# Optimization experiments

Measured on AMD Instinct MI355X. Metric: run time of the kernel, lower is better.

## Reference

```python
import jax, jax.numpy as jnp
import numpy as np

B, M, S, F, E, H, L = 4, 10, 1024, 128, 512, 8, 6
DH = E // H
NV, NP = 6, 3
LN_EPS = 1e-5


def _ln(x, g, b):
    mu = x.mean(-1, keepdims=True)
    var = ((x - mu) ** 2).mean(-1, keepdims=True)
    return (x - mu) * jax.lax.rsqrt(var + LN_EPS) * g + b


def setup_inputs() -> dict:
    key = jax.random.key(0)
    ks = jax.random.split(key, 24)
    sc = 0.02
    inp = {
        'features': jax.random.normal(ks[0], (B, M, S, F), jnp.float32),
        'target': jax.random.normal(ks[1], (B, S, NV), jnp.float32),
        'step_idx': jax.random.randint(ks[2], (B,), 0, 40),
        'day_of_year': jax.random.randint(ks[3], (B,), 0, 365),
        'emb_W': jax.random.normal(ks[4], (F, E), jnp.float32) * sc,
        'emb_b': jnp.zeros((E,), jnp.float32),
        'station_emb': jax.random.uniform(ks[5], (S + 1, E), jnp.float32),
        'Wq': jax.random.normal(ks[6], (L, E, E), jnp.float32) * sc,
        'Wk': jax.random.normal(ks[7], (L, E, E), jnp.float32) * sc,
        'Wv': jax.random.normal(ks[8], (L, E, E), jnp.float32) * sc,
        'attn_W': jax.random.normal(ks[9], (L, E, E), jnp.float32) * sc,
        'attn_b': jnp.zeros((L, E), jnp.float32),
        'ln_attn_g': jnp.ones((L, E), jnp.float32),
        'ln_attn_b': jnp.zeros((L, E), jnp.float32),
        'ffn_W1': jax.random.normal(ks[10], (L, E, E), jnp.float32) * sc,
        'ffn_b1': jnp.zeros((L, E), jnp.float32),
        'ffn_W2': jax.random.normal(ks[11], (L, E, E), jnp.float32) * sc,
        'ffn_b2': jnp.zeros((L, E), jnp.float32),
        'ln1_g': jnp.ones((L, E), jnp.float32),
        'ln1_b': jnp.zeros((L, E), jnp.float32),
        'ln2_g': jnp.ones((L, E), jnp.float32),
        'ln2_b': jnp.zeros((L, E), jnp.float32),
        'reg_W': jax.random.normal(ks[12], (E, NV * NP), jnp.float32) * sc,
        'reg_b': jnp.zeros((NV * NP,), jnp.float32),
    }
    return inp


def reference(features, target, step_idx, day_of_year, emb_W, emb_b, station_emb,
              Wq, Wk, Wv, attn_W, attn_b, ln_attn_g, ln_attn_b,
              ffn_W1, ffn_b1, ffn_W2, ffn_b2, ln1_g, ln1_b, ln2_g, ln2_b,
              reg_W, reg_b):
    # embedding + mean over ensemble members (select_member='mean')
    emb = features @ emb_W + emb_b            # [B,M,S,E]
    x = emb.mean(axis=1)                      # [B,S,E]

    # station embedding lookup; stations with any NaN target get index -1 (last row)
    sid = jnp.broadcast_to(jnp.arange(S), (B, S))
    has_no_obs = jnp.isnan(target).any(axis=-1)
    sid = jnp.where(has_no_obs, -1, sid)
    x = x + station_emb[sid]                  # [B,S,E]

    scale = jnp.sqrt(jnp.float32(DH))
    for i in range(L):
        # multi-head attention; NOTE: original softmax is over dim=0 (batch)
        q = (x @ Wq[i]).reshape(B, S, H, DH)
        k = (x @ Wk[i]).reshape(B, S, H, DH)
        v = (x @ Wv[i]).reshape(B, S, H, DH)
        att = jnp.einsum('bqhd,bkhd->hbqk', q, k) / scale   # [H,B,S,S]
        att = jax.nn.softmax(att, axis=1)                   # softmax over batch dim, per original
        o = jnp.einsum('hbqk,bkhd->bqhd', att, v).reshape(B, S, E)
        o = o @ attn_W[i] + attn_b[i]
        o = jax.nn.silu(_ln(o, ln_attn_g[i], ln_attn_b[i]))
        # block: LN -> FFN -> residual -> LN (dropout = 0)
        h = _ln(o, ln1_g[i], ln1_b[i])
        f = jax.nn.silu(h @ ffn_W1[i] + ffn_b1[i]) @ ffn_W2[i] + ffn_b2[i]
        x = _ln(f + h, ln2_g[i], ln2_b[i])

    out = x @ reg_W + reg_b                   # [B,S,NV*NP]
    return out.reshape(B, S, NV, NP)
```

## Files before the change

kernel.cpp:

```cpp
#include <hip/hip_runtime.h>
#include <stdint.h>

typedef float   f32x4 __attribute__((ext_vector_type(4)));
typedef float   f32x2 __attribute__((ext_vector_type(2)));
typedef __bf16  bfx8  __attribute__((ext_vector_type(8)));
typedef uint16_t u16x8 __attribute__((ext_vector_type(8)));
typedef uint16_t u16x4 __attribute__((ext_vector_type(4)));

#define AS1(p) ((__attribute__((address_space(1))) void*)(p))
#define AS3(p) ((__attribute__((address_space(3))) void*)(p))

__device__ __forceinline__ uint16_t f2bf(float f) {
    union { float f; uint32_t u; } c; c.f = f;
    uint32_t u = c.u;
    return (uint16_t)((u + 0x7FFFu + ((u >> 16) & 1u)) >> 16);
}
__device__ __forceinline__ float sigmoidf_(float x) { return 1.0f / (1.0f + __expf(-x)); }
__device__ __forceinline__ float frcp(float x) { float r; asm("v_rcp_f32 %0, %1" : "=v"(r) : "v"(x)); return r; }
__device__ __forceinline__ uint32_t cvtpk(float lo, float hi) {
    uint32_t r; asm("v_cvt_pk_bf16_f32 %0, %1, %2" : "=v"(r) : "v"(lo), "v"(hi)); return r;
}

__global__ __launch_bounds__(256) void wconv_k(
    const float* __restrict__ Wq, const float* __restrict__ Wk, const float* __restrict__ Wv,
    const float* __restrict__ Wo, const float* __restrict__ W1, const float* __restrict__ W2,
    const float* __restrict__ Wemb, uint16_t* __restrict__ arena)
{
    __shared__ uint16_t tl[64][65];
    const int z = blockIdx.z;
    const float* in; uint16_t* out; int K, N;
    if (z < 36) {
        const int type = z / 6, l = z % 6;
        const float* bases[6] = {Wq, Wk, Wv, Wo, W1, W2};
        in = bases[type] + (size_t)l * 512 * 512;
        K = 512; N = 512;
        if (type < 3) out = arena + (size_t)l * 786432u + (size_t)type * 262144u;
        else          out = arena + 4718592u + (size_t)(type - 3) * 1572864u + (size_t)l * 262144u;
    } else {
        if (blockIdx.y >= 2) return;
        in = Wemb; K = 128; N = 512;
        out = arena + 9437184u;
    }
    const int n0 = blockIdx.x * 64, k0 = blockIdx.y * 64;
    const int t = threadIdx.x, r = t >> 2, seg = t & 3;
    const float* src = in + (size_t)(k0 + r) * N + n0 + seg * 16;
#pragma unroll
    for (int v2 = 0; v2 < 4; ++v2) {
        f32x4 d = *(const f32x4*)(src + v2 * 4);
#pragma unroll
        for (int j = 0; j < 4; ++j) tl[r][seg * 16 + v2 * 4 + j] = f2bf(d[j]);
    }
    __syncthreads();
    u16x8 o0, o1;
#pragma unroll
    for (int j = 0; j < 8; ++j) { o0[j] = tl[seg * 16 + j][r]; o1[j] = tl[seg * 16 + 8 + j][r]; }
    uint16_t* dst = out + (size_t)(n0 + r) * K + k0 + seg * 16;
    *(u16x8*)dst = o0; *(u16x8*)(dst + 8) = o1;
}

__global__ __launch_bounds__(256) void fmean_k(const float* __restrict__ feat, uint16_t* __restrict__ fm)
{
    int id = blockIdx.x * 256 + threadIdx.x;
    int f = id & 127, row = id >> 7;
    int b = row >> 10, s = row & 1023;
    float acc = 0.f;
#pragma unroll
    for (int m = 0; m < 10; ++m)
        acc += feat[(size_t)((b * 10 + m) * 1024 + s) * 128 + f];
    fm[id] = f2bf(acc * 0.1f);
}

template<int BIAS, int SILU, int OUTBF, int KMOD, int STATION>
__global__ __launch_bounds__(256) void gemm64(const uint16_t* __restrict__ A,
    const uint16_t* __restrict__ Bw, const float* __restrict__ bias,
    void* __restrict__ Cout, int Msz, int Nsz, int Ksz,
    const float* __restrict__ target, const float* __restrict__ semb)
{
    __shared__ uint16_t lA[2][64 * 64];
    __shared__ uint16_t lB[2][64 * 64];
    const int t = threadIdx.x;
    const int lane = t & 63, w = t >> 6;
    const int wm = (w >> 1) * 32, wn = (w & 1) * 32;
    const int m0 = blockIdx.y * 64, n0 = blockIdx.x * 64;
    const int l15 = lane & 15, l4 = lane >> 4;
    const int srow = lane >> 3, sseg = lane & 7;

    auto stage = [&](int buf, int k0) {
        const size_t bstride = KMOD ? 512 : (size_t)Ksz;
        const int bk0 = KMOD ? (k0 & 511) : k0;
        char* lab = (char*)lA[buf]; char* lbb = (char*)lB[buf];
#pragma unroll
        for (int i = 0; i < 2; ++i) {
            int row = w * 16 + i * 8 + srow;
            const char* ga = (const char*)A + ((size_t)(m0 + row) * Ksz + k0) * 2 + sseg * 16;
            __builtin_amdgcn_global_load_lds(AS1(ga), AS3(lab + (w * 16 + i * 8) * 128), 16, 0, 0);
            const char* gb = (const char*)Bw + ((size_t)(n0 + row) * bstride + bk0) * 2 + sseg * 16;
            __builtin_amdgcn_global_load_lds(AS1(gb), AS3(lbb + (w * 16 + i * 8) * 128), 16, 0, 0);
        }
    };

    f32x4 acc[2][2] = {};
    const int nk = Ksz >> 6;
    stage(0, 0);
    __syncthreads();
    for (int i = 0; i < nk; ++i) {
        if (i + 1 < nk) stage((i + 1) & 1, (i + 1) * 64);
        const char* lab = (const char*)lA[i & 1];
        const char* lbb = (const char*)lB[i & 1];
#pragma unroll
        for (int kf = 0; kf < 2; ++kf) {
            bfx8 af[2], bf2[2];
#pragma unroll
            for (int mf = 0; mf < 2; ++mf)
                af[mf] = *(const bfx8*)(lab + (wm + mf * 16 + l15) * 128 + kf * 64 + l4 * 16);
#pragma unroll
            for (int nf = 0; nf < 2; ++nf)
                bf2[nf] = *(const bfx8*)(lbb + (wn + nf * 16 + l15) * 128 + kf * 64 + l4 * 16);
#pragma unroll
            for (int mf = 0; mf < 2; ++mf)
#pragma unroll
                for (int nf = 0; nf < 2; ++nf)
                    acc[mf][nf] = __builtin_amdgcn_mfma_f32_16x16x32_bf16(af[mf], bf2[nf], acc[mf][nf], 0, 0, 0);
        }
        __syncthreads();
    }
    if (STATION) {
#pragma unroll
        for (int mf = 0; mf < 2; ++mf)
#pragma unroll
            for (int r = 0; r < 4; ++r) {
                int row = m0 + wm + mf * 16 + l4 * 4 + r;
                int s = row & 1023;
                bool bad = false;
#pragma unroll
                for (int v = 0; v < 6; ++v) bad = bad || isnan(target[(size_t)row * 6 + v]);
                int sid = bad ? 1024 : s;
#pragma unroll
                for (int nf = 0; nf < 2; ++nf) {
                    int col = n0 + wn + nf * 16 + l15;
                    float val = acc[mf][nf][r] + bias[col] + semb[(size_t)sid * 512 + col];
                    ((uint16_t*)Cout)[(size_t)row * Nsz + col] = f2bf(val);
                }
            }
        return;
    }
#pragma unroll
    for (int mf = 0; mf < 2; ++mf)
#pragma unroll
        for (int nf = 0; nf < 2; ++nf)
#pragma unroll
            for (int r = 0; r < 4; ++r) {
                int row = m0 + wm + mf * 16 + l4 * 4 + r;
                int col = n0 + wn + nf * 16 + l15;
                float v = acc[mf][nf][r];
                if (BIAS) v += bias[col];
                if (SILU) v = v * sigmoidf_(v);
                if (OUTBF) ((uint16_t*)Cout)[(size_t)row * Nsz + col] = f2bf(v);
                else       ((float*)Cout)[(size_t)row * Nsz + col] = v;
            }
}

template<int VT>
__global__ __launch_bounds__(256) void gemm128(const uint16_t* __restrict__ A,
    const uint16_t* __restrict__ Bw, uint16_t* __restrict__ Cout, int Nsz, int Ksz,
    uint16_t* __restrict__ vtout)
{
    __shared__ uint16_t lA[2][128 * 64];
    __shared__ uint16_t lB[2][128 * 64];
    const int t = threadIdx.x;
    const int lane = t & 63, w = t >> 6;
    const int wm = (w >> 1) * 64, wn = (w & 1) * 64;
    const int m0 = blockIdx.y * 128, n0 = blockIdx.x * 128;
    const int l15 = lane & 15, l4 = lane >> 4;
    const int srow = lane >> 3, sseg = lane & 7;

    auto stage = [&](int buf, int k0) {
        char* lab = (char*)lA[buf]; char* lbb = (char*)lB[buf];
#pragma unroll
        for (int i = 0; i < 4; ++i) {
            int row = w * 32 + i * 8 + srow;
            const char* ga = (const char*)A + ((size_t)(m0 + row) * Ksz + k0) * 2 + sseg * 16;
            __builtin_amdgcn_global_load_lds(AS1(ga), AS3(lab + (w * 32 + i * 8) * 128), 16, 0, 0);
            const char* gb = (const char*)Bw + ((size_t)(n0 + row) * Ksz + k0) * 2 + sseg * 16;
            __builtin_amdgcn_global_load_lds(AS1(gb), AS3(lbb + (w * 32 + i * 8) * 128), 16, 0, 0);
        }
    };

    f32x4 acc[4][4] = {};
    const int nk = Ksz >> 6;
    stage(0, 0);
    __syncthreads();
    for (int i = 0; i < nk; ++i) {
        if (i + 1 < nk) stage((i + 1) & 1, (i + 1) * 64);
        const char* lab = (const char*)lA[i & 1];
        const char* lbb = (const char*)lB[i & 1];
#pragma unroll
        for (int kf = 0; kf < 2; ++kf) {
            bfx8 af[4], bf2[4];
#pragma unroll
            for (int mf = 0; mf < 4; ++mf)
                af[mf] = *(const bfx8*)(lab + (wm + mf * 16 + l15) * 128 + kf * 64 + l4 * 16);
#pragma unroll
            for (int nf = 0; nf < 4; ++nf)
                bf2[nf] = *(const bfx8*)(lbb + (wn + nf * 16 + l15) * 128 + kf * 64 + l4 * 16);
#pragma unroll
            for (int mf = 0; mf < 4; ++mf)
#pragma unroll
                for (int nf = 0; nf < 4; ++nf)
                    acc[mf][nf] = __builtin_amdgcn_mfma_f32_16x16x32_bf16(af[mf], bf2[nf], acc[mf][nf], 0, 0, 0);
        }
        __syncthreads();
    }
    if (VT && n0 >= 1024) {
#pragma unroll
        for (int mf = 0; mf < 4; ++mf)
#pragma unroll
            for (int nf = 0; nf < 4; ++nf) {
                int colv = n0 + wn + nf * 16 + l15 - 1024;
                int hh = colv >> 6, dh = colv & 63;
                int row = m0 + wm + mf * 16 + l4 * 4;
                int b = row >> 10, s = row & 1023;
                u16x4 ov;
#pragma unroll
                for (int r = 0; r < 4; ++r) ov[r] = f2bf(acc[mf][nf][r]);
                *(u16x4*)(vtout + (size_t)((b * 8 + hh) * 64 + dh) * 1024 + s) = ov;
            }
        return;
    }
#pragma unroll
    for (int mf = 0; mf < 4; ++mf)
#pragma unroll
        for (int nf = 0; nf < 4; ++nf)
#pragma unroll
            for (int r = 0; r < 4; ++r) {
                int row = m0 + wm + mf * 16 + l4 * 4 + r;
                int col = n0 + wn + nf * 16 + l15;
                Cout[(size_t)row * Nsz + col] = f2bf(acc[mf][nf][r]);
            }
}

__global__ __launch_bounds__(256, 2) void attn_k(const uint16_t* __restrict__ qkv,
    const uint16_t* __restrict__ vt, uint16_t* __restrict__ o16)
{
    __shared__ __align__(16) char lds[2][32768];
    const int t = threadIdx.x;
    const int lane = t & 63, w = t >> 6;
    const int l15 = lane & 15, l4 = lane >> 4;
    const int qsub = w & 1, kq = w >> 1;
    const int bid = blockIdx.x;
    const int h = bid & 7, qt = (bid >> 3) & 31, ks = bid >> 8;
    const int q0 = qt * 32 + qsub * 16;

    bfx8 qa[4][2];
#pragma unroll
    for (int b = 0; b < 4; ++b)
#pragma unroll
        for (int kf = 0; kf < 2; ++kf)
            qa[b][kf] = *(const bfx8*)(qkv + (size_t)(b * 1024 + q0 + l15) * 1536 + h * 64 + kf * 32 + l4 * 8);

    char* Kb = lds[kq];
    char* Vb = lds[kq] + 16384;

    auto stage = [&](int k0) {
#pragma unroll
        for (int j = 0; j < 8; ++j) {
            const int i = qsub * 8 + j;
            {
                int rho = i * 8 + (lane >> 3);
                int cd = (lane & 7) ^ (rho & 7);
                int b = rho >> 5, kl = rho & 31;
                const uint16_t* g = qkv + (size_t)(b * 1024 + k0 + kl) * 1536 + 512 + h * 64 + cd * 8;
                __builtin_amdgcn_global_load_lds(AS1(g), AS3(Kb + i * 1024), 16, 0, 0);
            }
            {
                int row = i * 16 + (lane >> 2);
                int cd = (lane & 3) ^ (row & 3);
                int b = row >> 6, d = row & 63;
                const uint16_t* g = vt + (size_t)((b * 8 + h) * 64 + d) * 1024 + k0 + cd * 8;
                __builtin_amdgcn_global_load_lds(AS1(g), AS3(Vb + i * 1024), 16, 0, 0);
            }
        }
    };

    f32x4 oacc[4][4] = {};
    const int kbase = ks * 512 + kq * 256;
    for (int tt = 0; tt < 8; ++tt) {
        stage(kbase + tt * 32);
        __syncthreads();
        f32x4 sacc[4][2] = {};
#pragma unroll
        for (int b = 0; b < 4; ++b)
#pragma unroll
            for (int kt = 0; kt < 2; ++kt) {
                int rho = b * 32 + kt * 16 + l15;
#pragma unroll
                for (int kf = 0; kf < 2; ++kf) {
                    int slot = (kf * 4 + l4) ^ (rho & 7);
                    bfx8 kb = *(const bfx8*)(Kb + rho * 128 + slot * 16);
                    sacc[b][kt] = __builtin_amdgcn_mfma_f32_16x16x32_bf16(kb, qa[b][kf], sacc[b][kt], 0, 0, 0);
                }
            }
        float p[2][4][4];
#pragma unroll
        for (int kt = 0; kt < 2; ++kt)
#pragma unroll
            for (int r = 0; r < 4; ++r) {
                float s0 = sacc[0][kt][r], s1 = sacc[1][kt][r];
                float s2 = sacc[2][kt][r], s3 = sacc[3][kt][r];
                float mx = fmaxf(fmaxf(s0, s1), fmaxf(s2, s3));
                float e0 = __expf((s0 - mx) * 0.125f);
                float e1 = __expf((s1 - mx) * 0.125f);
                float e2 = __expf((s2 - mx) * 0.125f);
                float e3 = __expf((s3 - mx) * 0.125f);
                float inv = frcp(e0 + e1 + e2 + e3);
                p[kt][0][r] = e0 * inv; p[kt][1][r] = e1 * inv;
                p[kt][2][r] = e2 * inv; p[kt][3][r] = e3 * inv;
            }
#pragma unroll
        for (int b = 0; b < 4; ++b) {
            union { uint32_t u[4]; bfx8 v; } pf;
            pf.u[0] = cvtpk(p[0][b][0], p[0][b][1]);
            pf.u[1] = cvtpk(p[0][b][2], p[0][b][3]);
            pf.u[2] = cvtpk(p[1][b][0], p[1][b][1]);
            pf.u[3] = cvtpk(p[1][b][2], p[1][b][3]);
#pragma unroll
            for (int m = 0; m < 4; ++m) {
                int row = b * 64 + m * 16 + l15;
                int c0 = ((l4 >> 1)) ^ (row & 3);
                int c1 = (2 + (l4 >> 1)) ^ (row & 3);
                u16x4 v0 = *(const u16x4*)(Vb + row * 64 + c0 * 16 + (l4 & 1) * 8);
                u16x4 v1 = *(const u16x4*)(Vb + row * 64 + c1 * 16 + (l4 & 1) * 8);
                union { u16x8 u; bfx8 v; } vf;
                vf.u = __builtin_shufflevector(v0, v1, 0, 1, 2, 3, 4, 5, 6, 7);
                oacc[b][m] = __builtin_amdgcn_mfma_f32_16x16x32_bf16(vf.v, pf.v, oacc[b][m], 0, 0, 0);
            }
        }
        __syncthreads();
    }
    float* cb = (float*)lds;
    if (kq == 1) {
#pragma unroll
        for (int b = 0; b < 4; ++b)
#pragma unroll
            for (int m = 0; m < 4; ++m)
                *(f32x4*)&cb[(qsub * 64 + lane) * 68 + (b * 4 + m) * 4] = oacc[b][m];
    }
    __syncthreads();
    if (kq == 0) {
#pragma unroll
        for (int b = 0; b < 4; ++b)
#pragma unroll
            for (int m = 0; m < 4; ++m) {
                f32x4 v = oacc[b][m] + *(const f32x4*)&cb[(qsub * 64 + lane) * 68 + (b * 4 + m) * 4];
                u16x4 ov;
#pragma unroll
                for (int r = 0; r < 4; ++r) ov[r] = f2bf(v[r]);
                *(u16x4*)(o16 + (size_t)(b * 1024 + q0 + l15) * 1024 + ks * 512 + h * 64 + m * 16 + 4 * l4) = ov;
            }
    }
}

__global__ __launch_bounds__(64) void ln_fuse_k(const float* __restrict__ in,
    const float* __restrict__ g1, const float* __restrict__ b1,
    const float* __restrict__ g2, const float* __restrict__ b2,
    float* __restrict__ h32, uint16_t* __restrict__ h16)
{
    const int row = blockIdx.x, lane = threadIdx.x;
    const float* p = in + (size_t)row * 512 + lane * 8;
    f32x4 a = *(const f32x4*)p, bvec = *(const f32x4*)(p + 4);
    float x[8] = {a[0], a[1], a[2], a[3], bvec[0], bvec[1], bvec[2], bvec[3]};
    float sum = 0.f, sq = 0.f;
#pragma unroll
    for (int i = 0; i < 8; ++i) { sum += x[i]; sq += x[i] * x[i]; }
    for (int m = 32; m; m >>= 1) { sum += __shfl_xor(sum, m); sq += __shfl_xor(sq, m); }
    float mu = sum * (1.f / 512.f);
    float rs = rsqrtf(sq * (1.f / 512.f) - mu * mu + 1e-5f);
    float y[8]; float s2 = 0.f, q2 = 0.f;
#pragma unroll
    for (int i = 0; i < 8; ++i) {
        int c = lane * 8 + i;
        float v = (x[i] - mu) * rs * g1[c] + b1[c];
        v = v * sigmoidf_(v);
        y[i] = v; s2 += v; q2 += v * v;
    }
    for (int m = 32; m; m >>= 1) { s2 += __shfl_xor(s2, m); q2 += __shfl_xor(q2, m); }
    float mu2 = s2 * (1.f / 512.f);
    float rs2 = rsqrtf(q2 * (1.f / 512.f) - mu2 * mu2 + 1e-5f);
#pragma unroll
    for (int i = 0; i < 8; ++i) {
        int c = lane * 8 + i;
        float v = (y[i] - mu2) * rs2 * g2[c] + b2[c];
        h32[(size_t)row * 512 + c] = v;
        h16[(size_t)row * 512 + c] = f2bf(v);
    }
}

template<int LAST>
__global__ __launch_bounds__(64) void ln_res_k(const float* __restrict__ f, const float* __restrict__ hres,
    const float* __restrict__ g, const float* __restrict__ bb, uint16_t* __restrict__ x16,
    const float* __restrict__ regW, const float* __restrict__ regb, float* __restrict__ out)
{
    const int row = blockIdx.x, lane = threadIdx.x;
    const size_t base = (size_t)row * 512 + lane * 8;
    f32x4 a = *(const f32x4*)(f + base), b2v = *(const f32x4*)(f + base + 4);
    f32x4 ha = *(const f32x4*)(hres + base), hb = *(const f32x4*)(hres + base + 4);
    float x[8] = {a[0] + ha[0], a[1] + ha[1], a[2] + ha[2], a[3] + ha[3],
                  b2v[0] + hb[0], b2v[1] + hb[1], b2v[2] + hb[2], b2v[3] + hb[3]};
    float sum = 0.f, sq = 0.f;
#pragma unroll
    for (int i = 0; i < 8; ++i) { sum += x[i]; sq += x[i] * x[i]; }
    for (int m = 32; m; m >>= 1) { sum += __shfl_xor(sum, m); sq += __shfl_xor(sq, m); }
    float mu = sum * (1.f / 512.f);
    float rs = rsqrtf(sq * (1.f / 512.f) - mu * mu + 1e-5f);
    float v[8];
#pragma unroll
    for (int i = 0; i < 8; ++i) {
        int c = lane * 8 + i;
        v[i] = (x[i] - mu) * rs * g[c] + bb[c];
    }
    if (!LAST) {
#pragma unroll
        for (int i = 0; i < 8; ++i) x16[base + i] = f2bf(v[i]);
    } else {
        float acc[18];
#pragma unroll
        for (int j = 0; j < 18; ++j) acc[j] = 0.f;
#pragma unroll
        for (int i = 0; i < 8; ++i) {
            const float* wr = regW + (size_t)(lane * 8 + i) * 18;
#pragma unroll
            for (int j = 0; j < 18; ++j) acc[j] += v[i] * wr[j];
        }
#pragma unroll
        for (int j = 0; j < 18; ++j) {
            acc[j] += __shfl_xor(acc[j], 1);
            acc[j] += __shfl_xor(acc[j], 2);
            acc[j] += __shfl_xor(acc[j], 4);
            acc[j] += __shfl_xor(acc[j], 8);
            acc[j] += __shfl_xor(acc[j], 16);
            acc[j] += __shfl_xor(acc[j], 32);
        }
        if (lane == 0) {
#pragma unroll
            for (int j = 0; j < 18; ++j)
                out[(size_t)row * 18 + j] = acc[j] + regb[j];
        }
    }
}

extern "C" void kernel_launch(void* const* d_in, const int* in_sizes, int n_in,
                              void* d_out, int out_size, void* d_ws, size_t ws_size,
                              hipStream_t stream)
{
    const float* features = (const float*)d_in[0];
    const float* target   = (const float*)d_in[1];
    const float* emb_W    = (const float*)d_in[4];
    const float* emb_b    = (const float*)d_in[5];
    const float* station  = (const float*)d_in[6];
    const float* Wq   = (const float*)d_in[7];
    const float* Wk   = (const float*)d_in[8];
    const float* Wv   = (const float*)d_in[9];
    const float* Wo   = (const float*)d_in[10];
    const float* attn_b = (const float*)d_in[11];
    const float* lng  = (const float*)d_in[12];
    const float* lnb  = (const float*)d_in[13];
    const float* W1   = (const float*)d_in[14];
    const float* b1   = (const float*)d_in[15];
    const float* W2   = (const float*)d_in[16];
    const float* b2   = (const float*)d_in[17];
    const float* ln1g = (const float*)d_in[18];
    const float* ln1b = (const float*)d_in[19];
    const float* ln2g = (const float*)d_in[20];
    const float* ln2b = (const float*)d_in[21];
    const float* regW = (const float*)d_in[22];
    const float* regb = (const float*)d_in[23];
    float* out = (float*)d_out;

    const size_t NEEDED = 73531392;
    if (ws_size < NEEDED) return;

    char* ws = (char*)d_ws;
    uint16_t* wt   = (uint16_t*)(ws);
    uint16_t* x16  = (uint16_t*)(ws + 19005440);
    uint16_t* qkv  = (uint16_t*)(ws + 23199744);
    uint16_t* vt   = (uint16_t*)(ws + 35782656);
    uint16_t* o16  = (uint16_t*)(ws + 39976960);
    float*    t32  = (float*)(ws + 48365568);
    float*    h32  = (float*)(ws + 56754176);
    uint16_t* h16  = (uint16_t*)(ws + 65142784);
    uint16_t* f16  = (uint16_t*)(ws + 69337088);
    uint16_t* fm16 = (uint16_t*)(ws + 56754176);

    wconv_k<<<dim3(8, 8, 37), 256, 0, stream>>>(Wq, Wk, Wv, Wo, W1, W2, emb_W, wt);
    fmean_k<<<dim3(2048), 256, 0, stream>>>(features, fm16);
    gemm64<1, 0, 1, 0, 1><<<dim3(8, 64), 256, 0, stream>>>(fm16, wt + 9437184u, emb_b, x16, 4096, 512, 128, target, station);

    for (int l = 0; l < 6; ++l) {
        gemm128<1><<<dim3(12, 32), 256, 0, stream>>>(x16, wt + (size_t)l * 786432u, qkv, 1536, 512, vt);
        attn_k<<<dim3(512), 256, 0, stream>>>(qkv, vt, o16);
        gemm64<1, 0, 0, 1, 0><<<dim3(8, 64), 256, 0, stream>>>(o16, wt + 4718592u + (size_t)l * 262144u, attn_b + l * 512, t32, 4096, 512, 1024, nullptr, nullptr);
        ln_fuse_k<<<dim3(4096), 64, 0, stream>>>(t32, lng + l * 512, lnb + l * 512, ln1g + l * 512, ln1b + l * 512, h32, h16);
        gemm64<1, 1, 1, 0, 0><<<dim3(8, 64), 256, 0, stream>>>(h16, wt + 6291456u + (size_t)l * 262144u, b1 + l * 512, f16, 4096, 512, 512, nullptr, nullptr);
        gemm64<1, 0, 0, 0, 0><<<dim3(8, 64), 256, 0, stream>>>(f16, wt + 7864320u + (size_t)l * 262144u, b2 + l * 512, t32, 4096, 512, 512, nullptr, nullptr);
        if (l < 5)
            ln_res_k<0><<<dim3(4096), 64, 0, stream>>>(t32, h32, ln2g + l * 512, ln2b + l * 512, x16, regW, regb, out);
        else
            ln_res_k<1><<<dim3(4096), 64, 0, stream>>>(t32, h32, ln2g + l * 512, ln2b + l * 512, x16, regW, regb, out);
    }
}
```

Measured before the change: 634.9 us.

## Prefetch next K/V tiles into LDS while computing current attention tile

The attention kernel's loop splits staging into separate K and V loaders. Each iteration first pulls its K and V fragments from LDS into registers, then issues the async global-to-LDS copy for the next tile, so the copy overlaps with the score MFMAs, the batch-axis softmax and the PV MFMAs. The goal is to hide global load latency that previously stalled every tile behind a barrier. In exchange, holding the K and V fragments in registers raises VGPR pressure and may reduce occupancy. Correctness also depends on the barriers waiting for the outstanding LDS-DMA copies before the buffers are read.

```diff
diff --git a/kernel.cpp b/kernel.cpp
--- a/kernel.cpp
+++ b/kernel.cpp
@@ -261,33 +261,36 @@
     char* Kb = lds[kq];
     char* Vb = lds[kq] + 16384;
 
-    auto stage = [&](int k0) {
+    auto stageK = [&](int k0) {
 #pragma unroll
         for (int j = 0; j < 8; ++j) {
             const int i = qsub * 8 + j;
-            {
-                int rho = i * 8 + (lane >> 3);
-                int cd = (lane & 7) ^ (rho & 7);
-                int b = rho >> 5, kl = rho & 31;
-                const uint16_t* g = qkv + (size_t)(b * 1024 + k0 + kl) * 1536 + 512 + h * 64 + cd * 8;
-                __builtin_amdgcn_global_load_lds(AS1(g), AS3(Kb + i * 1024), 16, 0, 0);
-            }
-            {
-                int row = i * 16 + (lane >> 2);
-                int cd = (lane & 3) ^ (row & 3);
-                int b = row >> 6, d = row & 63;
-                const uint16_t* g = vt + (size_t)((b * 8 + h) * 64 + d) * 1024 + k0 + cd * 8;
-                __builtin_amdgcn_global_load_lds(AS1(g), AS3(Vb + i * 1024), 16, 0, 0);
-            }
+            int rho = i * 8 + (lane >> 3);
+            int cd = (lane & 7) ^ (rho & 7);
+            int b = rho >> 5, kl = rho & 31;
+            const uint16_t* g = qkv + (size_t)(b * 1024 + k0 + kl) * 1536 + 512 + h * 64 + cd * 8;
+            __builtin_amdgcn_global_load_lds(AS1(g), AS3(Kb + i * 1024), 16, 0, 0);
+        }
+    };
+    auto stageV = [&](int k0) {
+#pragma unroll
+        for (int j = 0; j < 8; ++j) {
+            const int i = qsub * 8 + j;
+            int row = i * 16 + (lane >> 2);
+            int cd = (lane & 3) ^ (row & 3);
+            int b = row >> 6, d = row & 63;
+            const uint16_t* g = vt + (size_t)((b * 8 + h) * 64 + d) * 1024 + k0 + cd * 8;
+            __builtin_amdgcn_global_load_lds(AS1(g), AS3(Vb + i * 1024), 16, 0, 0);
         }
     };
 
     f32x4 oacc[4][4] = {};
     const int kbase = ks * 512 + kq * 256;
+    stageK(kbase); stageV(kbase);
+    __syncthreads();
     for (int tt = 0; tt < 8; ++tt) {
-        stage(kbase + tt * 32);
-        __syncthreads();
-        f32x4 sacc[4][2] = {};
+        const int k0n = kbase + (tt + 1) * 32;
+        bfx8 kbf[4][2][2];
 #pragma unroll
         for (int b = 0; b < 4; ++b)
 #pragma unroll
@@ -296,10 +299,19 @@
 #pragma unroll
                 for (int kf = 0; kf < 2; ++kf) {
                     int slot = (kf * 4 + l4) ^ (rho & 7);
-                    bfx8 kb = *(const bfx8*)(Kb + rho * 128 + slot * 16);
-                    sacc[b][kt] = __builtin_amdgcn_mfma_f32_16x16x32_bf16(kb, qa[b][kf], sacc[b][kt], 0, 0, 0);
+                    kbf[b][kt][kf] = *(const bfx8*)(Kb + rho * 128 + slot * 16);
                 }
             }
+        __syncthreads();
+        if (tt < 7) stageK(k0n);
+        f32x4 sacc[4][2] = {};
+#pragma unroll
+        for (int b = 0; b < 4; ++b)
+#pragma unroll
+            for (int kt = 0; kt < 2; ++kt)
+#pragma unroll
+                for (int kf = 0; kf < 2; ++kf)
+                    sacc[b][kt] = __builtin_amdgcn_mfma_f32_16x16x32_bf16(kbf[b][kt][kf], qa[b][kf], sacc[b][kt], 0, 0, 0);
         float p[2][4][4];
 #pragma unroll
         for (int kt = 0; kt < 2; ++kt)
@@ -316,13 +328,9 @@
                 p[kt][0][r] = e0 * inv; p[kt][1][r] = e1 * inv;
                 p[kt][2][r] = e2 * inv; p[kt][3][r] = e3 * inv;
             }
-#pragma unroll
-        for (int b = 0; b < 4; ++b) {
-            union { uint32_t u[4]; bfx8 v; } pf;
-            pf.u[0] = cvtpk(p[0][b][0], p[0][b][1]);
-            pf.u[1] = cvtpk(p[0][b][2], p[0][b][3]);
-            pf.u[2] = cvtpk(p[1][b][0], p[1][b][1]);
-            pf.u[3] = cvtpk(p[1][b][2], p[1][b][3]);
+        bfx8 vbf[4][4];
+#pragma unroll
+        for (int b = 0; b < 4; ++b)
 #pragma unroll
             for (int m = 0; m < 4; ++m) {
                 int row = b * 64 + m * 16 + l15;
@@ -332,10 +340,21 @@
                 u16x4 v1 = *(const u16x4*)(Vb + row * 64 + c1 * 16 + (l4 & 1) * 8);
                 union { u16x8 u; bfx8 v; } vf;
                 vf.u = __builtin_shufflevector(v0, v1, 0, 1, 2, 3, 4, 5, 6, 7);
-                oacc[b][m] = __builtin_amdgcn_mfma_f32_16x16x32_bf16(vf.v, pf.v, oacc[b][m], 0, 0, 0);
-            }
-        }
+                vbf[b][m] = vf.v;
+            }
         __syncthreads();
+        if (tt < 7) stageV(k0n);
+#pragma unroll
+        for (int b = 0; b < 4; ++b) {
+            union { uint32_t u[4]; bfx8 v; } pf;
+            pf.u[0] = cvtpk(p[0][b][0], p[0][b][1]);
+            pf.u[1] = cvtpk(p[0][b][2], p[0][b][3]);
+            pf.u[2] = cvtpk(p[1][b][0], p[1][b][1]);
+            pf.u[3] = cvtpk(p[1][b][2], p[1][b][3]);
+#pragma unroll
+            for (int m = 0; m < 4; ++m)
+                oacc[b][m] = __builtin_amdgcn_mfma_f32_16x16x32_bf16(vbf[b][m], pf.v, oacc[b][m], 0, 0, 0);
+        }
     }
     float* cb = (float*)lds;
     if (kq == 1) {
```

Result: no change. 637.6 us (+0.4%).
